# Performance work log

Hardware: AMD Instinct MI355X
Metric: run time of the kernel (lower is better)

Reference implementation:

```python
import jax, jax.numpy as jnp
import numpy as np

C, B, NZ, NGF, NC = 16, 2048, 100, 64, 512
DIMS = [NZ, NGF * 8, NGF * 4, NGF * 2, NGF * 4, NC]  # 100->512->256->128->256->512
EPS = 1e-5  # torch BatchNorm2d default


def setup_inputs() -> dict:
    key = jax.random.key(0)
    ks = jax.random.split(key, 6)
    inp = {"x": jax.random.normal(ks[0], (C, B, NZ, 1, 1), dtype=jnp.float32)}
    for l in range(5):  # 1x1 conv weights per class, stacked over class dim
        fan_in = DIMS[l]
        inp[f"W{l+1}"] = jax.random.normal(ks[1 + l], (C, DIMS[l + 1], DIMS[l]), dtype=jnp.float32) / np.float32(np.sqrt(fan_in))
        inp[f"b{l+1}"] = jnp.zeros((C, DIMS[l + 1]), dtype=jnp.float32)
    for l in range(4):  # BN affine params (torch init: weight=1, bias=0)
        inp[f"g{l+1}"] = jnp.ones((C, DIMS[l + 1]), dtype=jnp.float32)
        inp[f"be{l+1}"] = jnp.zeros((C, DIMS[l + 1]), dtype=jnp.float32)
    return inp


def _conv1x1(h, W, b):
    # h: [C,B,Fin], W: [C,Fout,Fin] -> [C,B,Fout]  (1x1 conv at H=W=1 == per-class GEMM)
    return jnp.einsum('cbi,coi->cbo', h, W) + b[:, None, :]


def _bn(h, g, b):
    # training-mode BatchNorm2d: biased batch stats over (B,H,W); here H=W=1 so over B
    mu = jnp.mean(h, axis=1, keepdims=True)
    var = jnp.mean((h - mu) ** 2, axis=1, keepdims=True)
    return g[:, None, :] * (h - mu) * jax.lax.rsqrt(var + EPS) + b[:, None, :]


def reference(x, W1, b1, W2, b2, W3, b3, W4, b4, W5, b5,
              g1, be1, g2, be2, g3, be3, g4, be4):
    h = x[..., 0, 0]  # [C,B,NZ] (1x1 spatial squeezed)
    h = jax.nn.relu(_bn(_conv1x1(h, W1, b1), g1, be1))
    h = jax.nn.relu(_bn(_conv1x1(h, W2, b2), g2, be2))
    h = jax.nn.relu(_bn(_conv1x1(h, W3, b3), g3, be3))
    h = jax.nn.relu(_bn(_conv1x1(h, W4, b4), g4, be4))
    h = _conv1x1(h, W5, b5)  # [C,B,NC]
    gendata = h.reshape(C * B, NC, 1, 1)  # concat over classes
    genlabel = jnp.repeat(jnp.arange(C, dtype=jnp.float32), B)
    return gendata, genlabel
```

## Files before the change

### kernel.cpp

```cpp
#include <hip/hip_runtime.h>
#include <hip/hip_bf16.h>
#include <math.h>

#define CCLS 16
#define BB   2048

using bf16x8 = __attribute__((ext_vector_type(8))) short;
using short8 = __attribute__((ext_vector_type(8))) short;
using f32x4  = __attribute__((ext_vector_type(4))) float;

__device__ __forceinline__ void split2(float e, short& hi, short& lo) {
    __hip_bfloat16 h = __float2bfloat16(e);
    hi = __builtin_bit_cast(short, h);
    lo = __builtin_bit_cast(short, __float2bfloat16(e - __bfloat162float(h)));
}

__device__ __forceinline__ void soft_barrier() {
    asm volatile("s_waitcnt lgkmcnt(0)" ::: "memory");
    __builtin_amdgcn_s_barrier();
    asm volatile("" ::: "memory");
}


struct PackDesc {
    const float* src[5];
    int nrt[5];
    int ksn[5];
    int kreal[5];
    int beg[6];
};

__global__ __launch_bounds__(256)
void pack_kernel(PackDesc d, char* __restrict__ base)
{
    const int bid = blockIdx.x;
    int s = 0;
    #pragma unroll
    for (int i = 0; i < 4; ++i) s += (bid >= d.beg[i + 1]);
    const int t    = bid - d.beg[s];
    const int ksn  = d.ksn[s], nrt = d.nrt[s], kreal = d.kreal[s];
    const int perc = nrt * ksn;
    const int c  = t / perc;
    const int r  = t - c * perc;
    const int rt = r / ksn;
    const int ks = r - rt * ksn;
    const float* src = d.src[s] + ((size_t)(c * nrt + rt) * 128) * kreal;
    char* dst = base + (size_t)bid * 16384;
    const int tid = threadIdx.x;

    #pragma unroll
    for (int it = 0; it < 2; ++it) {
        const int row = (tid >> 2) + (it << 6);
        const int cc  = tid & 3;
        const int q   = ((row >> 4) << 10) | (cc << 8) | ((row & 15) << 4);
        const int k0  = ks * 32 + cc * 8;
        const float* sp = src + (size_t)row * kreal + k0;
        float e[8];
        if (k0 + 8 <= kreal) {
            float4 v0 = *(const float4*)sp;
            float4 v1 = *(const float4*)(sp + 4);
            e[0]=v0.x; e[1]=v0.y; e[2]=v0.z; e[3]=v0.w;
            e[4]=v1.x; e[5]=v1.y; e[6]=v1.z; e[7]=v1.w;
        } else {
            #pragma unroll
            for (int j = 0; j < 8; ++j) e[j] = (k0 + j < kreal) ? sp[j] : 0.f;
        }
        short hv[8], lv[8];
        #pragma unroll
        for (int j = 0; j < 8; ++j) split2(e[j], hv[j], lv[j]);
        *(short8*)(dst + q)        = (short8){hv[0],hv[1],hv[2],hv[3],hv[4],hv[5],hv[6],hv[7]};
        *(short8*)(dst + 8192 + q) = (short8){lv[0],lv[1],lv[2],lv[3],lv[4],lv[5],lv[6],lv[7]};
    }
}

template<int BM, int K, bool FUSE_BN, bool WRITE_STATS>
__global__ __launch_bounds__(256, 2)
void gemm4_kernel(const float* __restrict__ A, const char* __restrict__ Wpk,
                  const float* __restrict__ bias,
                  const float* __restrict__ psumIn, const float* __restrict__ psqIn,
                  const float* __restrict__ gIn, const float* __restrict__ beIn,
                  float* __restrict__ Out,
                  float* __restrict__ psumOut, float* __restrict__ psqOut,
                  const int Fout, const int nbtIn)
{
    constexpr int KS    = (K + 31) / 32;
    constexpr int PLANE = BM * 64;
    constexpr int BUF   = PLANE * 2;
    constexpr int MI    = BM / 32;
    constexpr int NV    = BM / 32;

    __shared__ __align__(16) char sm[2 * BUF + 4096];
    float* scs = (float*)(sm + 2 * BUF);
    float* shs = scs + 512;

    const int tid   = threadIdx.x;
    const int btile = blockIdx.x, otile = blockIdx.y, c = blockIdx.z;

    if (FUSE_BN) {
        for (int f = tid; f < K; f += 256) {
            const float* ps = psumIn + ((size_t)c * K + f) * nbtIn;
            const float* pq = psqIn  + ((size_t)c * K + f) * nbtIn;
            float s = 0.f, q = 0.f;
            for (int t = 0; t < nbtIn; t += 4) {
                float4 a4 = *(const float4*)(ps + t);
                float4 b4 = *(const float4*)(pq + t);
                s += (a4.x + a4.y) + (a4.z + a4.w);
                q += (b4.x + b4.y) + (b4.z + b4.w);
            }
            const float mean = s * (1.f / BB);
            const float var  = q * (1.f / BB) - mean * mean;
            const float rstd = rsqrtf(var + 1e-5f);
            const float scv  = gIn[(size_t)c * K + f] * rstd;
            scs[f] = scv;
            shs[f] = fmaf(-mean, scv, beIn[(size_t)c * K + f]);
        }
        __syncthreads();
    }

    const int b0 = btile * BM, o0 = otile * 128;
    const int OT = Fout >> 7;
    const char* wbase = Wpk + (size_t)((c * OT + otile) * KS) * 16384;

    const int arow = (BM == 128) ? (tid >> 1) : (tid >> 2);
    const int asub = (BM == 128) ? (tid & 1)  : (tid & 3);
    const int ak0  = (BM == 128) ? (asub << 4) : (asub << 3);
    const int kch  = (BM == 128) ? (asub << 1) : asub;
    const int awr  = ((arow >> 4) << 10) | (kch << 8) | ((arow & 15) << 4);
    const float* Arow = A + ((size_t)c * BB + b0 + arow) * K;

    const int lane = tid & 63, wv = tid >> 6;
    const int fr = lane & 15, fkc = lane >> 4;
    const int wrow = (BM == 128) ? ((wv >> 1) << 6) : ((wv >> 1) << 5);
    const int wcol = (wv & 1) << 6;
    const int wrg = wrow >> 4, wcg = wcol >> 4;

    auto loadA = [&](float4* av, int gk0) {
        #pragma unroll
        for (int i = 0; i < NV; ++i) {
            const int gk = gk0 + (i << 2);
            if constexpr ((K & 31) != 0) {
                if (gk + 4 <= K) av[i] = *(const float4*)(Arow + gk);
                else {
                    av[i].x = (gk + 0 < K) ? Arow[gk + 0] : 0.f;
                    av[i].y = (gk + 1 < K) ? Arow[gk + 1] : 0.f;
                    av[i].z = (gk + 2 < K) ? Arow[gk + 2] : 0.f;
                    av[i].w = (gk + 3 < K) ? Arow[gk + 3] : 0.f;
                }
            } else {
                av[i] = *(const float4*)(Arow + gk);
            }
        }
    };
    auto loadW = [&](bf16x8* w, int ks) {
        const char* wt = wbase + (size_t)ks * 16384;
        #pragma unroll
        for (int i = 0; i < 4; ++i) {
            const int wo = ((wcg + i) << 10) | (fkc << 8) | (fr << 4);
            w[i]     = *(const bf16x8*)(wt + wo);
            w[4 + i] = *(const bf16x8*)(wt + 8192 + wo);
        }
    };
    auto cvtStore = [&](char* dstbase, const float4* a, int gk0) {
        float e[NV * 4];
        #pragma unroll
        for (int i = 0; i < NV; ++i) {
            e[i*4+0] = a[i].x; e[i*4+1] = a[i].y; e[i*4+2] = a[i].z; e[i*4+3] = a[i].w;
        }
        if constexpr (FUSE_BN) {
            #pragma unroll
            for (int i = 0; i < NV; ++i) {
                const float4 sc = *(const float4*)(scs + gk0 + (i << 2));
                const float4 sh = *(const float4*)(shs + gk0 + (i << 2));
                e[i*4+0] = fmaxf(0.f, fmaf(e[i*4+0], sc.x, sh.x));
                e[i*4+1] = fmaxf(0.f, fmaf(e[i*4+1], sc.y, sh.y));
                e[i*4+2] = fmaxf(0.f, fmaf(e[i*4+2], sc.z, sh.z));
                e[i*4+3] = fmaxf(0.f, fmaf(e[i*4+3], sc.w, sh.w));
            }
        }
        short h[NV*4], l[NV*4];
        #pragma unroll
        for (int j = 0; j < NV*4; ++j) split2(e[j], h[j], l[j]);
        *(short8*)(dstbase + awr)         = (short8){h[0],h[1],h[2],h[3],h[4],h[5],h[6],h[7]};
        *(short8*)(dstbase + PLANE + awr) = (short8){l[0],l[1],l[2],l[3],l[4],l[5],l[6],l[7]};
        if constexpr (NV == 4) {
            *(short8*)(dstbase + awr + 256)         = (short8){h[8],h[9],h[10],h[11],h[12],h[13],h[14],h[15]};
            *(short8*)(dstbase + PLANE + awr + 256) = (short8){l[8],l[9],l[10],l[11],l[12],l[13],l[14],l[15]};
        }
    };

    f32x4 acc[MI][4];
    #pragma unroll
    for (int mi = 0; mi < MI; ++mi)
        #pragma unroll
        for (int ni = 0; ni < 4; ++ni)
            acc[mi][ni] = (f32x4){0.f, 0.f, 0.f, 0.f};

    bf16x8 wc[8], wn[8];

    {
        float4 av[NV];
        loadA(av, ak0);
        loadW(wc, 0);
        cvtStore(sm, av, ak0);
    }
    soft_barrier();

    #pragma unroll 2
    for (int ks = 0; ks < KS; ++ks) {
        const int cb = (ks & 1) ? BUF : 0;
        const int nb = cb ^ BUF;
        const bool hn = (ks + 1) < KS;

        float4 avn[NV];
        if (hn) {
            loadA(avn, ((ks + 1) << 5) + ak0);
            loadW(wn, ks + 1);
        }

        bf16x8 ah[MI], al[MI];
        #pragma unroll
        for (int i = 0; i < MI; ++i) {
            const int ao = ((wrg + i) << 10) | (fkc << 8) | (fr << 4);
            ah[i] = *(const bf16x8*)(sm + cb + ao);
            al[i] = *(const bf16x8*)(sm + cb + PLANE + ao);
        }
        #pragma unroll
        for (int mi = 0; mi < MI; ++mi)
            #pragma unroll
            for (int ni = 0; ni < 4; ++ni) {
                acc[mi][ni] = __builtin_amdgcn_mfma_f32_16x16x32_bf16(ah[mi], wc[ni],     acc[mi][ni], 0, 0, 0);
                acc[mi][ni] = __builtin_amdgcn_mfma_f32_16x16x32_bf16(ah[mi], wc[4 + ni], acc[mi][ni], 0, 0, 0);
                acc[mi][ni] = __builtin_amdgcn_mfma_f32_16x16x32_bf16(al[mi], wc[ni],     acc[mi][ni], 0, 0, 0);
            }

        if (hn) cvtStore(sm + nb, avn, ((ks + 1) << 5) + ak0);
        soft_barrier();
        if (hn) {
            #pragma unroll
            for (int i = 0; i < 8; ++i) wc[i] = wn[i];
        }
    }

    float bv[4];
    #pragma unroll
    for (int ni = 0; ni < 4; ++ni)
        bv[ni] = bias[(size_t)c * Fout + o0 + wcol + (ni << 4) + fr];

    float p[4] = {}, q[4] = {};
    const int rsub = (lane >> 4) << 2;
    #pragma unroll
    for (int mi = 0; mi < MI; ++mi) {
        #pragma unroll
        for (int j = 0; j < 4; ++j) {
            const int row = b0 + wrow + (mi << 4) + rsub + j;
            float* op = Out + ((size_t)c * BB + row) * Fout + o0 + wcol;
            #pragma unroll
            for (int ni = 0; ni < 4; ++ni) {
                const float v = acc[mi][ni][j] + bv[ni];
                op[(ni << 4) + fr] = v;
                if (WRITE_STATS) { p[ni] += v; q[ni] += v * v; }
            }
        }
    }

    if (WRITE_STATS) {
        #pragma unroll
        for (int ni = 0; ni < 4; ++ni) {
            p[ni] += __shfl_xor(p[ni], 16); p[ni] += __shfl_xor(p[ni], 32);
            q[ni] += __shfl_xor(q[ni], 16); q[ni] += __shfl_xor(q[ni], 32);
        }
        float* redp = (float*)sm;
        float* redq = (float*)(sm + 1024);
        if (lane < 16) {
            const int base = (wv >> 1) * 128 + wcol;
            #pragma unroll
            for (int ni = 0; ni < 4; ++ni) {
                redp[base + (ni << 4) + fr] = p[ni];
                redq[base + (ni << 4) + fr] = q[ni];
            }
        }
        __syncthreads();
        if (tid < 128) {
            const float sp = redp[tid] + redp[128 + tid];
            const float sq = redq[tid] + redq[128 + tid];
            const size_t o = ((size_t)c * Fout + o0 + tid) * gridDim.x + btile;
            psumOut[o] = sp;
            psqOut[o]  = sq;
        }
    }
}

__global__ __launch_bounds__(256)
void label_kernel(float* __restrict__ out)
{
    const int i = blockIdx.x * 256 + threadIdx.x;
    out[i] = (float)(i >> 11);
}

extern "C" void kernel_launch(void* const* d_in, const int* in_sizes, int n_in,
                              void* d_out, int out_size, void* d_ws, size_t ws_size,
                              hipStream_t stream)
{
    const float* x = (const float*)d_in[0];
    const float* W[5];  const float* bs[5];
    for (int l = 0; l < 5; ++l) { W[l] = (const float*)d_in[1 + 2 * l]; bs[l] = (const float*)d_in[2 + 2 * l]; }
    const float* g[4];  const float* be[4];
    for (int l = 0; l < 4; ++l) { g[l] = (const float*)d_in[11 + 2 * l]; be[l] = (const float*)d_in[12 + 2 * l]; }

    float* out     = (float*)d_out;
    float* gendata = out;
    float* label   = out + (size_t)CCLS * BB * 512;

    float* ws  = (float*)d_ws;
    float* h2  = ws;
    float* h3  = h2 + 8388608;
    float* h4  = h2;
    float* ps1 = h3 + 4194304;
    float* pq1 = ps1 + 131072;
    float* ps2 = pq1 + 131072;
    float* pq2 = ps2 + 65536;
    float* ps3 = pq2 + 65536;
    float* pq3 = ps3 + 65536;
    float* ps4 = pq3 + 65536;
    float* pq4 = ps4 + 65536;
    char*  pack = (char*)(pq4 + 65536);

    const char* wpk1 = pack;
    const char* wpk2 = pack + (size_t)256  * 16384;
    const char* wpk3 = pack + (size_t)768  * 16384;
    const char* wpk4 = pack + (size_t)896  * 16384;
    const char* wpk5 = pack + (size_t)1024 * 16384;

    const dim3 blk(256);

    PackDesc pd;
    pd.src[0] = W[0]; pd.src[1] = W[1]; pd.src[2] = W[2]; pd.src[3] = W[3]; pd.src[4] = W[4];
    const int nrt[5]   = {4, 2, 1, 2, 4};
    const int ksn[5]   = {4, 16, 8, 4, 8};
    const int kreal[5] = {100, 512, 256, 128, 256};
    const int beg[6]   = {0, 256, 768, 896, 1024, 1536};
    for (int i = 0; i < 5; ++i) { pd.nrt[i] = nrt[i]; pd.ksn[i] = ksn[i]; pd.kreal[i] = kreal[i]; }
    for (int i = 0; i < 6; ++i) pd.beg[i] = beg[i];
    pack_kernel<<<dim3(1536), blk, 0, stream>>>(pd, pack);

    gemm4_kernel<128, 100, false, true><<<dim3(16, 4, CCLS), blk, 0, stream>>>(
        x, wpk1, bs[0], nullptr, nullptr, nullptr, nullptr,
        gendata, ps1, pq1, 512, 0);

    gemm4_kernel<128, 512, true, true><<<dim3(16, 2, CCLS), blk, 0, stream>>>(
        gendata, wpk2, bs[1], ps1, pq1, g[0], be[0],
        h2, ps2, pq2, 256, 16);

    gemm4_kernel<64, 256, true, true><<<dim3(32, 1, CCLS), blk, 0, stream>>>(
        h2, wpk3, bs[2], ps2, pq2, g[1], be[1],
        h3, ps3, pq3, 128, 16);

    gemm4_kernel<128, 128, true, true><<<dim3(16, 2, CCLS), blk, 0, stream>>>(
        h3, wpk4, bs[3], ps3, pq3, g[2], be[2],
        h4, ps4, pq4, 256, 32);

    gemm4_kernel<128, 256, true, false><<<dim3(16, 4, CCLS), blk, 0, stream>>>(
        h4, wpk5, bs[4], ps4, pq4, g[3], be[3],
        gendata, nullptr, nullptr, 512, 16);

    label_kernel<<<dim3(CCLS * BB / 256), blk, 0, stream>>>(label);
}
```

Before: 154.9 us.

## Triple-buffer A tiles with two-ahead prefetch and retile layer 4 GEMM

Changes the GEMM main loop from double to triple LDS buffering. A-tile global loads are now issued two k-steps ahead and the weight loads are deferred until after the LDS reads. MFMA sections are wrapped in s_setprio to favour the matrix work. Layer 4 moves to a 64-row tile with twice as many blocks, so the BN partial-stat buffers double in size and layer 5 reads 32 partials. This costs more LDS and registers per block, which may reduce occupancy.

```diff
diff --git a/kernel.cpp b/kernel.cpp
--- a/kernel.cpp
+++ b/kernel.cpp
@@ -75,7 +75,7 @@
 
 template<int BM, int K, bool FUSE_BN, bool WRITE_STATS>
 __global__ __launch_bounds__(256, 2)
-void gemm4_kernel(const float* __restrict__ A, const char* __restrict__ Wpk,
+void gemm5_kernel(const float* __restrict__ A, const char* __restrict__ Wpk,
                   const float* __restrict__ bias,
                   const float* __restrict__ psumIn, const float* __restrict__ psqIn,
                   const float* __restrict__ gIn, const float* __restrict__ beIn,
@@ -88,10 +88,11 @@
     constexpr int BUF   = PLANE * 2;
     constexpr int MI    = BM / 32;
     constexpr int NV    = BM / 32;
-
-    __shared__ __align__(16) char sm[2 * BUF + 4096];
-    float* scs = (float*)(sm + 2 * BUF);
-    float* shs = scs + 512;
+    constexpr int TBL   = FUSE_BN ? (2 * K * 4) : 256;
+
+    __shared__ __align__(16) char sm[3 * BUF + TBL];
+    float* scs = (float*)(sm + 3 * BUF);
+    float* shs = scs + (FUSE_BN ? K : 0);
 
     const int tid   = threadIdx.x;
     const int btile = blockIdx.x, otile = blockIdx.y, c = blockIdx.z;
@@ -196,26 +197,23 @@
             acc[mi][ni] = (f32x4){0.f, 0.f, 0.f, 0.f};
 
     bf16x8 wc[8], wn[8];
+    float4 avP[NV], avQ[NV];
 
     {
-        float4 av[NV];
-        loadA(av, ak0);
+        float4 av0[NV];
+        loadA(av0, ak0);
+        if (KS > 1) loadA(avP, 32 + ak0);
         loadW(wc, 0);
-        cvtStore(sm, av, ak0);
+        cvtStore(sm, av0, ak0);
     }
     soft_barrier();
 
     #pragma unroll 2
     for (int ks = 0; ks < KS; ++ks) {
-        const int cb = (ks & 1) ? BUF : 0;
-        const int nb = cb ^ BUF;
-        const bool hn = (ks + 1) < KS;
-
-        float4 avn[NV];
-        if (hn) {
-            loadA(avn, ((ks + 1) << 5) + ak0);
-            loadW(wn, ks + 1);
-        }
+        const int cb = (ks % 3) * BUF;
+        const int nb = ((ks + 1) % 3) * BUF;
+        const bool hn  = (ks + 1) < KS;
+        const bool hn2 = (ks + 2) < KS;
 
         bf16x8 ah[MI], al[MI];
         #pragma unroll
@@ -224,6 +222,11 @@
             ah[i] = *(const bf16x8*)(sm + cb + ao);
             al[i] = *(const bf16x8*)(sm + cb + PLANE + ao);
         }
+
+        if (hn2) loadA(avQ, ((ks + 2) << 5) + ak0);
+        if (hn)  loadW(wn, ks + 1);
+
+        __builtin_amdgcn_s_setprio(1);
         #pragma unroll
         for (int mi = 0; mi < MI; ++mi)
             #pragma unroll
@@ -232,12 +235,16 @@
                 acc[mi][ni] = __builtin_amdgcn_mfma_f32_16x16x32_bf16(ah[mi], wc[4 + ni], acc[mi][ni], 0, 0, 0);
                 acc[mi][ni] = __builtin_amdgcn_mfma_f32_16x16x32_bf16(al[mi], wc[ni],     acc[mi][ni], 0, 0, 0);
             }
-
-        if (hn) cvtStore(sm + nb, avn, ((ks + 1) << 5) + ak0);
+        __builtin_amdgcn_s_setprio(0);
+
+        if (hn) cvtStore(sm + nb, avP, ((ks + 1) << 5) + ak0);
+
         soft_barrier();
         if (hn) {
             #pragma unroll
             for (int i = 0; i < 8; ++i) wc[i] = wn[i];
+            #pragma unroll
+            for (int i = 0; i < NV; ++i) avP[i] = avQ[i];
         }
     }
 
@@ -322,8 +329,8 @@
     float* ps3 = pq2 + 65536;
     float* pq3 = ps3 + 65536;
     float* ps4 = pq3 + 65536;
-    float* pq4 = ps4 + 65536;
-    char*  pack = (char*)(pq4 + 65536);
+    float* pq4 = ps4 + 131072;
+    char*  pack = (char*)(pq4 + 131072);
 
     const char* wpk1 = pack;
     const char* wpk2 = pack + (size_t)256  * 16384;
@@ -343,25 +350,25 @@
     for (int i = 0; i < 6; ++i) pd.beg[i] = beg[i];
     pack_kernel<<<dim3(1536), blk, 0, stream>>>(pd, pack);
 
-    gemm4_kernel<128, 100, false, true><<<dim3(16, 4, CCLS), blk, 0, stream>>>(
+    gemm5_kernel<128, 100, false, true><<<dim3(16, 4, CCLS), blk, 0, stream>>>(
         x, wpk1, bs[0], nullptr, nullptr, nullptr, nullptr,
         gendata, ps1, pq1, 512, 0);
 
-    gemm4_kernel<128, 512, true, true><<<dim3(16, 2, CCLS), blk, 0, stream>>>(
+    gemm5_kernel<128, 512, true, true><<<dim3(16, 2, CCLS), blk, 0, stream>>>(
         gendata, wpk2, bs[1], ps1, pq1, g[0], be[0],
         h2, ps2, pq2, 256, 16);
 
-    gemm4_kernel<64, 256, true, true><<<dim3(32, 1, CCLS), blk, 0, stream>>>(
+    gemm5_kernel<64, 256, true, true><<<dim3(32, 1, CCLS), blk, 0, stream>>>(
         h2, wpk3, bs[2], ps2, pq2, g[1], be[1],
         h3, ps3, pq3, 128, 16);
 
-    gemm4_kernel<128, 128, true, true><<<dim3(16, 2, CCLS), blk, 0, stream>>>(
+    gemm5_kernel<64, 128, true, true><<<dim3(32, 2, CCLS), blk, 0, stream>>>(
         h3, wpk4, bs[3], ps3, pq3, g[2], be[2],
         h4, ps4, pq4, 256, 32);
 
-    gemm4_kernel<128, 256, true, false><<<dim3(16, 4, CCLS), blk, 0, stream>>>(
+    gemm5_kernel<128, 256, true, false><<<dim3(16, 4, CCLS), blk, 0, stream>>>(
         h4, wpk5, bs[4], ps4, pq4, g[3], be[3],
-        gendata, nullptr, nullptr, 512, 16);
+        gendata, nullptr, nullptr, 512, 32);
 
     label_kernel<<<dim3(CCLS * BB / 256), blk, 0, stream>>>(label);
 }
```

Result: slower. 174.2 us (+12.5%).
